# Optimization experiments

Hardware: AMD Instinct MI355X
Metric: run time of the kernel (lower is better)

The kernel has to match this reference:

```python
import jax, jax.numpy as jnp
import numpy as np

B, S, D = 32, 2048, 1024


def setup_inputs() -> dict:
    key = jax.random.key(0)
    k = jax.random.split(key, 7)
    midi_features = jax.random.normal(k[0], (B, S, D), dtype=jnp.float32)
    scale_id = jax.random.randint(k[1], (B,), 0, 3)
    midi_mask = jax.random.randint(k[2], (B, S), 0, 2).astype(jnp.int32)
    # Stacked branch params: index 0=high, 1=mid, 2=low (matches SCALE_TO_ID)
    W = jax.random.normal(k[3], (3, D, D), dtype=jnp.float32) * 0.02  # Linear weight (out,in)
    b = jax.random.normal(k[4], (3, D), dtype=jnp.float32) * 0.02
    scale_embed = jax.random.normal(k[5], (3, D), dtype=jnp.float32) * 0.02
    branch_embed = jax.random.normal(k[6], (3, D), dtype=jnp.float32) * 0.02
    return {"midi_features": midi_features, "scale_id": scale_id, "midi_mask": midi_mask,
            "W": W, "b": b, "scale_embed": scale_embed, "branch_embed": branch_embed}


def reference(midi_features, scale_id, midi_mask, W, b, scale_embed, branch_embed):
    # Per-sample scale routing: gather the branch's Linear weight for each sample
    # (equivalent to the torch fancy-indexing scatter into out[idx]).
    Wb = W[scale_id]               # (B, D, D) torch Linear convention: y = x @ W.T + b
    bb = b[scale_id]               # (B, D)
    out = jax.nn.silu(jnp.einsum('bsd,bed->bse', midi_features, Wb) + bb[:, None, :])
    # Dropout is identity in eval mode.
    out = out + scale_embed[scale_id][:, None, :]       # (B, S, D)

    seq_mask = midi_mask > 0                             # (B, S) bool
    w = seq_mask.astype(out.dtype)[:, :, None]           # (B, S, 1)
    denom = jnp.maximum(w.sum(axis=1), 1e-6)             # (B, 1)
    low_vec = (out * w).sum(axis=1) / denom              # (B, D) masked mean

    high_cond = out + branch_embed[0]                    # (B, S, D)
    mid_cond = out + branch_embed[1]                     # (B, S, D)
    low_cond = low_vec[:, None, :] + branch_embed[2]     # (B, 1, D) weak_low_alignment=True
    return high_cond, mid_cond, low_cond
```

## Files before the change

### kernel.cpp

```cpp
#include <hip/hip_runtime.h>
#include <hip/hip_bf16.h>

#define B_ 32
#define S_ 2048
#define D_ 1024
#define BM 128
#define BN 128
#define BK 64
#define NK (D_ / BK)

typedef __attribute__((ext_vector_type(8))) short bf16x8;
typedef __attribute__((ext_vector_type(4))) float f32x4;
typedef __attribute__((ext_vector_type(4))) float float4v;

#define AS1 __attribute__((address_space(1)))
#define AS3 __attribute__((address_space(3)))

__device__ __forceinline__ short f2bf(float f) {
    union { float f; unsigned u; } uf;
    uf.f = f;
    unsigned u = uf.u;
    u += 0x7FFFu + ((u >> 16) & 1u);
    return (short)(u >> 16);
}

__global__ __launch_bounds__(256) void cvt_bf16(const float4v* __restrict__ src,
                                                bf16x8* __restrict__ dst, int n8) {
    const int stride = gridDim.x * blockDim.x;
    for (int i = blockIdx.x * blockDim.x + threadIdx.x; i < n8; i += stride) {
        float4v a = src[2 * i], b = src[2 * i + 1];
        bf16x8 v;
#pragma unroll
        for (int j = 0; j < 4; ++j) {
            v[j]     = f2bf(a[j]);
            v[4 + j] = f2bf(b[j]);
        }
        dst[i] = v;
    }
}

__global__ __launch_bounds__(256, 2) void fused_gemm_bf16(
    const __hip_bfloat16* __restrict__ aBf,
    const __hip_bfloat16* __restrict__ wBf,
    const int*   __restrict__ scale_id,
    const int*   __restrict__ mask,
    const float* __restrict__ bias,
    const float* __restrict__ scemb,
    const float* __restrict__ bremb,
    float*       __restrict__ out,
    float*       __restrict__ colws)
{
    __shared__ __align__(16) short As[2][BM * BK];
    __shared__ __align__(16) short Bs[2][BM * BK];

    const int tid = threadIdx.x;
    const int lane = tid & 63;
    const int wid = tid >> 6;

    const int NTI = D_ / BN;
    const int MTI = S_ / BM;
    const int NWG = B_ * MTI * NTI;
    const int CPX = NWG / 8;
    int lid = ((int)blockIdx.x % 8) * CPX + ((int)blockIdx.x / 8);
    int nt = lid % NTI;
    int mt = (lid / NTI) % MTI;
    int bb = lid / (NTI * MTI);

    const int sid = scale_id[bb];

    const __hip_bfloat16* aBase = aBf + ((size_t)bb * S_ + (size_t)mt * BM) * D_;
    const __hip_bfloat16* bBase = wBf + ((size_t)sid * D_ + (size_t)nt * BN) * D_;

    const int l3 = lane >> 3;
    const int cb = (lane & 7) * 16;

    auto stage = [&](int buf, int kt) {
#pragma unroll
        for (int c = 0; c < 4; ++c) {
            const int seg = c * 4 + wid;
            const int row = seg * 8 + l3;
            const int scb = cb ^ ((row & 7) << 4);
            const __hip_bfloat16* ga = aBase + (size_t)row * D_ + kt * BK + (scb >> 1);
            const __hip_bfloat16* gb = bBase + (size_t)row * D_ + kt * BK + (scb >> 1);
            __builtin_amdgcn_global_load_lds((const AS1 unsigned int*)ga,
                (AS3 unsigned int*)&As[buf][seg * 512], 16, 0, 0);
            __builtin_amdgcn_global_load_lds((const AS1 unsigned int*)gb,
                (AS3 unsigned int*)&Bs[buf][seg * 512], 16, 0, 0);
        }
    };

    f32x4 acc[4][4];
#pragma unroll
    for (int mi = 0; mi < 4; ++mi)
#pragma unroll
        for (int ni = 0; ni < 4; ++ni)
            acc[mi][ni] = (f32x4){0.f, 0.f, 0.f, 0.f};

    const int wm = wid >> 1, wn = wid & 1;
    const int fr = lane & 15;
    const int fg = lane >> 4;

    stage(0, 0);
    asm volatile("s_waitcnt vmcnt(0)" ::: "memory");
    __syncthreads();

    int buf = 0;
    for (int kt = 0; kt < NK; ++kt) {
        if (kt + 1 < NK) stage(buf ^ 1, kt + 1);
#pragma unroll
        for (int kk = 0; kk < 2; ++kk) {
            bf16x8 af[4], bfr[4];
#pragma unroll
            for (int mi = 0; mi < 4; ++mi) {
                const int row = wm * 64 + mi * 16 + fr;
                const int byt = row * 128 + ((kk * 64 + fg * 16) ^ ((fr & 7) << 4));
                af[mi] = *(const bf16x8*)((const char*)&As[buf][0] + byt);
            }
#pragma unroll
            for (int ni = 0; ni < 4; ++ni) {
                const int row = wn * 64 + ni * 16 + fr;
                const int byt = row * 128 + ((kk * 64 + fg * 16) ^ ((fr & 7) << 4));
                bfr[ni] = *(const bf16x8*)((const char*)&Bs[buf][0] + byt);
            }
#pragma unroll
            for (int mi = 0; mi < 4; ++mi)
#pragma unroll
                for (int ni = 0; ni < 4; ++ni)
                    acc[mi][ni] = __builtin_amdgcn_mfma_f32_16x16x32_bf16(
                        af[mi], bfr[ni], acc[mi][ni], 0, 0, 0);
        }
        asm volatile("s_waitcnt vmcnt(0)" ::: "memory");
        __syncthreads();
        buf ^= 1;
    }

    const int ncolbase = nt * BN + wn * 64;
    float bv[4], sv[4];
#pragma unroll
    for (int ni = 0; ni < 4; ++ni) {
        const int n = ncolbase + ni * 16 + fr;
        bv[ni] = bias[sid * D_ + n];
        sv[ni] = scemb[sid * D_ + n];
    }

    float colsum[4] = {0.f, 0.f, 0.f, 0.f};
#pragma unroll
    for (int mi = 0; mi < 4; ++mi) {
        const int mrow0 = mt * BM + wm * 64 + mi * 16 + fg * 4;
        float mk[4];
#pragma unroll
        for (int r = 0; r < 4; ++r)
            mk[r] = (mask[(size_t)bb * S_ + mrow0 + r] > 0) ? 1.f : 0.f;
#pragma unroll
        for (int ni = 0; ni < 4; ++ni) {
#pragma unroll
            for (int r = 0; r < 4; ++r) {
                const float v = acc[mi][ni][r] + bv[ni];
                const float o = v / (1.f + __expf(-v)) + sv[ni];
                acc[mi][ni][r] = o;
                colsum[ni] += mk[r] * o;
            }
        }
    }

#pragma unroll
    for (int ni = 0; ni < 4; ++ni) {
        float s = colsum[ni];
        s += __shfl_xor(s, 16);
        s += __shfl_xor(s, 32);
        if (fg == 0)
            atomicAdd(&colws[(size_t)bb * D_ + (ncolbase + ni * 16 + fr)], s);
    }

    float* ldsF = (float*)&As[0][0];
    const int lrowR = tid >> 3;
    const int c8 = tid & 7;

    float4v b0q[4], b1q[4];
#pragma unroll
    for (int q = 0; q < 4; ++q) {
        const int gcol = nt * BN + (c8 + q * 8) * 4;
        b0q[q] = *(const float4v*)&bremb[0 * D_ + gcol];
        b1q[q] = *(const float4v*)&bremb[1 * D_ + gcol];
    }

    const size_t MIDOFF = (size_t)B_ * S_ * D_;

#pragma unroll
    for (int mi = 0; mi < 4; ++mi) {
#pragma unroll
        for (int ni = 0; ni < 4; ++ni)
#pragma unroll
            for (int r = 0; r < 4; ++r)
                ldsF[(wm * 16 + fg * 4 + r) * 132 + wn * 64 + ni * 16 + fr] =
                    acc[mi][ni][r];
        __syncthreads();

        const int grow = mt * BM + (lrowR >> 4) * 64 + mi * 16 + (lrowR & 15);
        const size_t rowbase = ((size_t)bb * S_ + grow) * D_ + nt * BN;
#pragma unroll
        for (int q = 0; q < 4; ++q) {
            const int c4 = c8 + q * 8;
            float4v v = *(const float4v*)&ldsF[lrowR * 132 + c4 * 4];
            float4v h = v + b0q[q];
            float4v m = v + b1q[q];
            __builtin_nontemporal_store(h, (float4v*)&out[rowbase + c4 * 4]);
            __builtin_nontemporal_store(m, (float4v*)&out[MIDOFF + rowbase + c4 * 4]);
        }
        __syncthreads();
    }
}

__global__ __launch_bounds__(256, 2) void fused_gemm_f32(
    const float* __restrict__ midi,
    const int*   __restrict__ scale_id,
    const int*   __restrict__ mask,
    const float* __restrict__ W,
    const float* __restrict__ bias,
    const float* __restrict__ scemb,
    const float* __restrict__ bremb,
    float*       __restrict__ out,
    float*       __restrict__ ws)
{
    __shared__ __align__(16) short As[BM * BK];
    __shared__ __align__(16) short Bs[BM * BK];

    const int tid = threadIdx.x;
    const int NTI = D_ / BN;
    const int MTI = S_ / BM;
    const int NWG = B_ * MTI * NTI;
    const int CPX = NWG / 8;
    int lid = ((int)blockIdx.x % 8) * CPX + ((int)blockIdx.x / 8);
    int nt = lid % NTI;
    int mt = (lid / NTI) % MTI;
    int bb = lid / (NTI * MTI);

    const int sid = scale_id[bb];
    const float* aBase = midi + ((size_t)bb * S_ + (size_t)mt * BM) * D_;
    const float* bBase = W + ((size_t)sid * D_ + (size_t)nt * BN) * D_;

    const int r0 = tid >> 3;
    const int kp = (tid & 7) * 8;

    float4v aL[4], aH[4], bL[4], bH[4];

    auto load_regs = [&](int kt) {
        const int kc = kt * BK + kp;
#pragma unroll
        for (int i = 0; i < 4; ++i) {
            const float* pa = aBase + (size_t)(r0 + 32 * i) * D_ + kc;
            aL[i] = *(const float4v*)pa;
            aH[i] = *(const float4v*)(pa + 4);
            const float* pb = bBase + (size_t)(r0 + 32 * i) * D_ + kc;
            bL[i] = *(const float4v*)pb;
            bH[i] = *(const float4v*)(pb + 4);
        }
    };

    auto write_lds = [&]() {
#pragma unroll
        for (int i = 0; i < 4; ++i) {
            const int row = r0 + 32 * i;
            const int off = (row * BK + kp) ^ ((row & 7) << 3);
            bf16x8 va, vb;
#pragma unroll
            for (int j = 0; j < 4; ++j) {
                va[j]     = f2bf(aL[i][j]);
                va[4 + j] = f2bf(aH[i][j]);
                vb[j]     = f2bf(bL[i][j]);
                vb[4 + j] = f2bf(bH[i][j]);
            }
            *(bf16x8*)&As[off] = va;
            *(bf16x8*)&Bs[off] = vb;
        }
    };

    f32x4 acc[4][4];
#pragma unroll
    for (int mi = 0; mi < 4; ++mi)
#pragma unroll
        for (int ni = 0; ni < 4; ++ni)
            acc[mi][ni] = (f32x4){0.f, 0.f, 0.f, 0.f};

    const int lane = tid & 63;
    const int wid = tid >> 6;
    const int wm = wid >> 1, wn = wid & 1;
    const int fr = lane & 15;
    const int fg = lane >> 4;

    load_regs(0);
    write_lds();
    __syncthreads();

    for (int kt = 0; kt < NK; ++kt) {
        if (kt + 1 < NK) load_regs(kt + 1);
#pragma unroll
        for (int kk = 0; kk < 2; ++kk) {
            bf16x8 af[4], bfr[4];
#pragma unroll
            for (int mi = 0; mi < 4; ++mi) {
                const int row = wm * 64 + mi * 16 + fr;
                const int off = (row * BK + kk * 32 + fg * 8) ^ ((row & 7) << 3);
                af[mi] = *(const bf16x8*)&As[off];
            }
#pragma unroll
            for (int ni = 0; ni < 4; ++ni) {
                const int row = wn * 64 + ni * 16 + fr;
                const int off = (row * BK + kk * 32 + fg * 8) ^ ((row & 7) << 3);
                bfr[ni] = *(const bf16x8*)&Bs[off];
            }
#pragma unroll
            for (int mi = 0; mi < 4; ++mi)
#pragma unroll
                for (int ni = 0; ni < 4; ++ni)
                    acc[mi][ni] = __builtin_amdgcn_mfma_f32_16x16x32_bf16(
                        af[mi], bfr[ni], acc[mi][ni], 0, 0, 0);
        }
        __syncthreads();
        if (kt + 1 < NK) write_lds();
        __syncthreads();
    }

    const int ncolbase = nt * BN + wn * 64;
    float bv[4], sv[4], b0v[4], b1v[4];
#pragma unroll
    for (int ni = 0; ni < 4; ++ni) {
        const int n = ncolbase + ni * 16 + fr;
        bv[ni]  = bias[sid * D_ + n];
        sv[ni]  = scemb[sid * D_ + n];
        b0v[ni] = bremb[0 * D_ + n];
        b1v[ni] = bremb[1 * D_ + n];
    }

    const size_t MIDOFF = (size_t)B_ * S_ * D_;
    float colsum[4] = {0.f, 0.f, 0.f, 0.f};

#pragma unroll
    for (int mi = 0; mi < 4; ++mi) {
        const int mrow0 = mt * BM + wm * 64 + mi * 16 + fg * 4;
        float mk[4];
#pragma unroll
        for (int r = 0; r < 4; ++r)
            mk[r] = (mask[(size_t)bb * S_ + mrow0 + r] > 0) ? 1.f : 0.f;
#pragma unroll
        for (int ni = 0; ni < 4; ++ni) {
            const int n = ncolbase + ni * 16 + fr;
#pragma unroll
            for (int r = 0; r < 4; ++r) {
                const float v = acc[mi][ni][r] + bv[ni];
                const float o = v / (1.f + __expf(-v)) + sv[ni];
                const size_t idx = ((size_t)bb * S_ + (size_t)(mrow0 + r)) * D_ + n;
                __builtin_nontemporal_store(o + b0v[ni], &out[idx]);
                __builtin_nontemporal_store(o + b1v[ni], &out[MIDOFF + idx]);
                colsum[ni] += mk[r] * o;
            }
        }
    }

#pragma unroll
    for (int ni = 0; ni < 4; ++ni) {
        float s = colsum[ni];
        s += __shfl_xor(s, 16);
        s += __shfl_xor(s, 32);
        if (fg == 0)
            atomicAdd(&ws[(size_t)bb * D_ + (ncolbase + ni * 16 + fr)], s);
    }
}

__global__ void finalize(const int* __restrict__ mask,
                         const float* __restrict__ ws,
                         const float* __restrict__ bremb,
                         float* __restrict__ out)
{
    const int b = blockIdx.x;
    const int tid = threadIdx.x;

    int c = 0;
    for (int s = tid; s < S_; s += 256)
        c += (mask[(size_t)b * S_ + s] > 0) ? 1 : 0;
#pragma unroll
    for (int m = 1; m < 64; m <<= 1)
        c += __shfl_xor(c, m);

    __shared__ int part[4];
    if ((tid & 63) == 0) part[tid >> 6] = c;
    __syncthreads();
    const float denom = fmaxf((float)(part[0] + part[1] + part[2] + part[3]), 1e-6f);
    const float inv = 1.f / denom;

    const size_t LOWOFF = (size_t)2 * B_ * S_ * D_;
    for (int e = tid; e < D_; e += 256)
        out[LOWOFF + (size_t)b * D_ + e] = ws[(size_t)b * D_ + e] * inv + bremb[2 * D_ + e];
}

extern "C" void kernel_launch(void* const* d_in, const int* in_sizes, int n_in,
                              void* d_out, int out_size, void* d_ws, size_t ws_size,
                              hipStream_t stream) {
    const float* midi     = (const float*)d_in[0];
    const int*   scale_id = (const int*)d_in[1];
    const int*   mask     = (const int*)d_in[2];
    const float* W        = (const float*)d_in[3];
    const float* bias     = (const float*)d_in[4];
    const float* scemb    = (const float*)d_in[5];
    const float* bremb    = (const float*)d_in[6];
    float* out = (float*)d_out;
    float* colws = (float*)d_ws;

    const size_t COLWS_B = (size_t)B_ * D_ * sizeof(float);
    const size_t WBF_B   = (size_t)3 * D_ * D_ * sizeof(short);
    const size_t ABF_B   = (size_t)B_ * S_ * D_ * sizeof(short);
    const size_t need    = COLWS_B + WBF_B + ABF_B;

    hipMemsetAsync(colws, 0, COLWS_B, stream);

    if (ws_size >= need) {
        __hip_bfloat16* wBf = (__hip_bfloat16*)((char*)d_ws + COLWS_B);
        __hip_bfloat16* aBf = (__hip_bfloat16*)((char*)d_ws + COLWS_B + WBF_B);
        cvt_bf16<<<dim3(2048), dim3(256), 0, stream>>>(
            (const float4v*)midi, (bf16x8*)aBf, (B_ * S_ * D_) / 8);
        cvt_bf16<<<dim3(512), dim3(256), 0, stream>>>(
            (const float4v*)W, (bf16x8*)wBf, (3 * D_ * D_) / 8);
        fused_gemm_bf16<<<dim3(B_ * (S_ / BM) * (D_ / BN)), dim3(256), 0, stream>>>(
            aBf, wBf, scale_id, mask, bias, scemb, bremb, out, colws);
    } else {
        fused_gemm_f32<<<dim3(B_ * (S_ / BM) * (D_ / BN)), dim3(256), 0, stream>>>(
            midi, scale_id, mask, W, bias, scemb, bremb, out, colws);
    }

    finalize<<<dim3(B_), dim3(256), 0, stream>>>(mask, colws, bremb, out);
}
```

Before: 382.5 us.

## Enlarge bf16 GEMM tile to 256x256 with 8 waves and half-tile staging pipeline

```diff
diff --git a/kernel.cpp b/kernel.cpp
--- a/kernel.cpp
+++ b/kernel.cpp
@@ -4,10 +4,11 @@
 #define B_ 32
 #define S_ 2048
 #define D_ 1024
-#define BM 128
-#define BN 128
+
+#define BM 256
+#define BN 256
 #define BK 64
-#define NK (D_ / BK)
+#define NKT (D_ / BK)
 
 typedef __attribute__((ext_vector_type(8))) short bf16x8;
 typedef __attribute__((ext_vector_type(4))) float f32x4;
@@ -39,7 +40,7 @@
     }
 }
 
-__global__ __launch_bounds__(256, 2) void fused_gemm_bf16(
+__global__ __launch_bounds__(512, 2) void fused_gemm_bf16(
     const __hip_bfloat16* __restrict__ aBf,
     const __hip_bfloat16* __restrict__ wBf,
     const int*   __restrict__ scale_id,
@@ -56,6 +57,8 @@
     const int tid = threadIdx.x;
     const int lane = tid & 63;
     const int wid = tid >> 6;
+    const int wm = wid >> 2;
+    const int wn = wid & 3;
 
     const int NTI = D_ / BN;
     const int MTI = S_ / BM;
@@ -67,119 +70,150 @@
     int bb = lid / (NTI * MTI);
 
     const int sid = scale_id[bb];
-
     const __hip_bfloat16* aBase = aBf + ((size_t)bb * S_ + (size_t)mt * BM) * D_;
     const __hip_bfloat16* bBase = wBf + ((size_t)sid * D_ + (size_t)nt * BN) * D_;
 
-    const int l3 = lane >> 3;
-    const int cb = (lane & 7) * 16;
-
-    auto stage = [&](int buf, int kt) {
-#pragma unroll
-        for (int c = 0; c < 4; ++c) {
-            const int seg = c * 4 + wid;
-            const int row = seg * 8 + l3;
-            const int scb = cb ^ ((row & 7) << 4);
-            const __hip_bfloat16* ga = aBase + (size_t)row * D_ + kt * BK + (scb >> 1);
-            const __hip_bfloat16* gb = bBase + (size_t)row * D_ + kt * BK + (scb >> 1);
-            __builtin_amdgcn_global_load_lds((const AS1 unsigned int*)ga,
-                (AS3 unsigned int*)&As[buf][seg * 512], 16, 0, 0);
-            __builtin_amdgcn_global_load_lds((const AS1 unsigned int*)gb,
-                (AS3 unsigned int*)&Bs[buf][seg * 512], 16, 0, 0);
+    const int lrow8 = lane >> 3;
+    const int scb = ((lane & 7) * 16) ^ (lrow8 << 4);
+
+    auto stageA = [&](int nb, int h, int kt) {
+#pragma unroll
+        for (int j = 0; j < 2; ++j) {
+            const int base = h * 128 + j * 64 + wid * 8;
+            const int grow = j * 128 + h * 64 + wid * 8 + lrow8;
+            const __hip_bfloat16* g = aBase + (size_t)grow * D_ + kt * BK + (scb >> 1);
+            __builtin_amdgcn_global_load_lds((const AS1 unsigned int*)g,
+                (AS3 unsigned int*)&As[nb][base * 64], 16, 0, 0);
         }
     };
-
-    f32x4 acc[4][4];
-#pragma unroll
-    for (int mi = 0; mi < 4; ++mi)
+    auto stageB = [&](int nb, int h, int kt) {
+#pragma unroll
+        for (int j = 0; j < 2; ++j) {
+            const int base = h * 128 + j * 64 + wid * 8;
+            const int grow = base + lrow8;
+            const __hip_bfloat16* g = bBase + (size_t)grow * D_ + kt * BK + (scb >> 1);
+            __builtin_amdgcn_global_load_lds((const AS1 unsigned int*)g,
+                (AS3 unsigned int*)&Bs[nb][base * 64], 16, 0, 0);
+        }
+    };
+
+    const int fr = lane & 15;
+    const int fg = lane >> 4;
+
+    f32x4 acc[8][4];
+#pragma unroll
+    for (int mi = 0; mi < 8; ++mi)
 #pragma unroll
         for (int ni = 0; ni < 4; ++ni)
             acc[mi][ni] = (f32x4){0.f, 0.f, 0.f, 0.f};
 
-    const int wm = wid >> 1, wn = wid & 1;
-    const int fr = lane & 15;
-    const int fg = lane >> 4;
-
-    stage(0, 0);
-    asm volatile("s_waitcnt vmcnt(0)" ::: "memory");
+    auto compute = [&](int cur, int mh, int bh) {
+        bf16x8 af[4][2], bv[2][2];
+#pragma unroll
+        for (int mi = 0; mi < 4; ++mi) {
+            const int l = mh * 128 + wm * 64 + mi * 16 + fr;
+            const int rb = l * 128;
+#pragma unroll
+            for (int kk = 0; kk < 2; ++kk) {
+                const int byt = rb + ((kk * 64 + fg * 16) ^ ((l & 7) << 4));
+                af[mi][kk] = *(const bf16x8*)((const char*)&As[cur][0] + byt);
+            }
+        }
+#pragma unroll
+        for (int ni = 0; ni < 2; ++ni) {
+            const int l = bh * 128 + wn * 32 + ni * 16 + fr;
+            const int rb = l * 128;
+#pragma unroll
+            for (int kk = 0; kk < 2; ++kk) {
+                const int byt = rb + ((kk * 64 + fg * 16) ^ ((l & 7) << 4));
+                bv[ni][kk] = *(const bf16x8*)((const char*)&Bs[cur][0] + byt);
+            }
+        }
+        __builtin_amdgcn_s_setprio(1);
+#pragma unroll
+        for (int mi = 0; mi < 4; ++mi)
+#pragma unroll
+            for (int ni = 0; ni < 2; ++ni)
+#pragma unroll
+                for (int kk = 0; kk < 2; ++kk)
+                    acc[mh * 4 + mi][bh * 2 + ni] = __builtin_amdgcn_mfma_f32_16x16x32_bf16(
+                        af[mi][kk], bv[ni][kk], acc[mh * 4 + mi][bh * 2 + ni], 0, 0, 0);
+        __builtin_amdgcn_s_setprio(0);
+    };
+
+#define PWAIT() do { \
+    asm volatile("s_waitcnt vmcnt(6)" ::: "memory"); \
+    asm volatile("s_barrier" ::: "memory"); } while (0)
+
+    stageB(0, 0, 0); stageA(0, 0, 0); stageB(0, 1, 0); stageA(0, 1, 0);
+
+    for (int kt = 0; kt < NKT; kt += 2) {
+        const int k1 = kt + 1;
+        const int k1n = (k1 + 1 < NKT) ? k1 + 1 : k1;
+        stageB(1, 0, k1);  PWAIT(); compute(0, 0, 0);
+        stageA(1, 0, k1);  PWAIT(); compute(0, 0, 1);
+        stageB(1, 1, k1);  PWAIT(); compute(0, 1, 0);
+        stageA(1, 1, k1);  PWAIT(); compute(0, 1, 1);
+        stageB(0, 0, k1n); PWAIT(); compute(1, 0, 0);
+        stageA(0, 0, k1n); PWAIT(); compute(1, 0, 1);
+        stageB(0, 1, k1n); PWAIT(); compute(1, 1, 0);
+        stageA(0, 1, k1n); PWAIT(); compute(1, 1, 1);
+    }
+#undef PWAIT
+
     __syncthreads();
 
-    int buf = 0;
-    for (int kt = 0; kt < NK; ++kt) {
-        if (kt + 1 < NK) stage(buf ^ 1, kt + 1);
-#pragma unroll
-        for (int kk = 0; kk < 2; ++kk) {
-            bf16x8 af[4], bfr[4];
-#pragma unroll
-            for (int mi = 0; mi < 4; ++mi) {
-                const int row = wm * 64 + mi * 16 + fr;
-                const int byt = row * 128 + ((kk * 64 + fg * 16) ^ ((fr & 7) << 4));
-                af[mi] = *(const bf16x8*)((const char*)&As[buf][0] + byt);
-            }
-#pragma unroll
-            for (int ni = 0; ni < 4; ++ni) {
-                const int row = wn * 64 + ni * 16 + fr;
-                const int byt = row * 128 + ((kk * 64 + fg * 16) ^ ((fr & 7) << 4));
-                bfr[ni] = *(const bf16x8*)((const char*)&Bs[buf][0] + byt);
-            }
-#pragma unroll
-            for (int mi = 0; mi < 4; ++mi)
-#pragma unroll
-                for (int ni = 0; ni < 4; ++ni)
-                    acc[mi][ni] = __builtin_amdgcn_mfma_f32_16x16x32_bf16(
-                        af[mi], bfr[ni], acc[mi][ni], 0, 0, 0);
-        }
-        asm volatile("s_waitcnt vmcnt(0)" ::: "memory");
-        __syncthreads();
-        buf ^= 1;
-    }
-
-    const int ncolbase = nt * BN + wn * 64;
-    float bv[4], sv[4];
-#pragma unroll
-    for (int ni = 0; ni < 4; ++ni) {
-        const int n = ncolbase + ni * 16 + fr;
-        bv[ni] = bias[sid * D_ + n];
-        sv[ni] = scemb[sid * D_ + n];
-    }
-
-    float colsum[4] = {0.f, 0.f, 0.f, 0.f};
-#pragma unroll
-    for (int mi = 0; mi < 4; ++mi) {
-        const int mrow0 = mt * BM + wm * 64 + mi * 16 + fg * 4;
+    const int colb = nt * BN;
+    float bv2[2][2], sv2[2][2];
+#pragma unroll
+    for (int bh = 0; bh < 2; ++bh)
+#pragma unroll
+        for (int ni = 0; ni < 2; ++ni) {
+            const int n = colb + bh * 128 + wn * 32 + ni * 16 + fr;
+            bv2[bh][ni] = bias[sid * D_ + n];
+            sv2[bh][ni] = scemb[sid * D_ + n];
+        }
+
+    float colsum[2][2] = {{0.f, 0.f}, {0.f, 0.f}};
+#pragma unroll
+    for (int mig = 0; mig < 8; ++mig) {
+        const int mrow0 = mt * BM + wm * 128 + mig * 16 + fg * 4;
         float mk[4];
 #pragma unroll
         for (int r = 0; r < 4; ++r)
             mk[r] = (mask[(size_t)bb * S_ + mrow0 + r] > 0) ? 1.f : 0.f;
 #pragma unroll
-        for (int ni = 0; ni < 4; ++ni) {
-#pragma unroll
-            for (int r = 0; r < 4; ++r) {
-                const float v = acc[mi][ni][r] + bv[ni];
-                const float o = v / (1.f + __expf(-v)) + sv[ni];
-                acc[mi][ni][r] = o;
-                colsum[ni] += mk[r] * o;
-            }
-        }
-    }
-
-#pragma unroll
-    for (int ni = 0; ni < 4; ++ni) {
-        float s = colsum[ni];
-        s += __shfl_xor(s, 16);
-        s += __shfl_xor(s, 32);
-        if (fg == 0)
-            atomicAdd(&colws[(size_t)bb * D_ + (ncolbase + ni * 16 + fr)], s);
-    }
+        for (int bh = 0; bh < 2; ++bh)
+#pragma unroll
+            for (int ni = 0; ni < 2; ++ni)
+#pragma unroll
+                for (int r = 0; r < 4; ++r) {
+                    const float v = acc[mig][bh * 2 + ni][r] + bv2[bh][ni];
+                    const float o = v / (1.f + __expf(-v)) + sv2[bh][ni];
+                    acc[mig][bh * 2 + ni][r] = o;
+                    colsum[bh][ni] += mk[r] * o;
+                }
+    }
+
+#pragma unroll
+    for (int bh = 0; bh < 2; ++bh)
+#pragma unroll
+        for (int ni = 0; ni < 2; ++ni) {
+            float s = colsum[bh][ni];
+            s += __shfl_xor(s, 16);
+            s += __shfl_xor(s, 32);
+            if (fg == 0)
+                atomicAdd(&colws[(size_t)bb * D_ + (colb + bh * 128 + wn * 32 + ni * 16 + fr)], s);
+        }
 
     float* ldsF = (float*)&As[0][0];
-    const int lrowR = tid >> 3;
-    const int c8 = tid & 7;
+    const int lr = tid >> 4;
+    const int cg = tid & 15;
 
     float4v b0q[4], b1q[4];
 #pragma unroll
     for (int q = 0; q < 4; ++q) {
-        const int gcol = nt * BN + (c8 + q * 8) * 4;
+        const int gcol = colb + cg * 16 + q * 4;
         b0q[q] = *(const float4v*)&bremb[0 * D_ + gcol];
         b1q[q] = *(const float4v*)&bremb[1 * D_ + gcol];
     }
@@ -187,29 +221,36 @@
     const size_t MIDOFF = (size_t)B_ * S_ * D_;
 
 #pragma unroll
-    for (int mi = 0; mi < 4; ++mi) {
-#pragma unroll
-        for (int ni = 0; ni < 4; ++ni)
-#pragma unroll
-            for (int r = 0; r < 4; ++r)
-                ldsF[(wm * 16 + fg * 4 + r) * 132 + wn * 64 + ni * 16 + fr] =
-                    acc[mi][ni][r];
+    for (int mig = 0; mig < 8; ++mig) {
+#pragma unroll
+        for (int bh = 0; bh < 2; ++bh)
+#pragma unroll
+            for (int ni = 0; ni < 2; ++ni)
+#pragma unroll
+                for (int r = 0; r < 4; ++r)
+                    ldsF[(wm * 16 + fg * 4 + r) * 260 + bh * 128 + wn * 32 + ni * 16 + fr] =
+                        acc[mig][bh * 2 + ni][r];
         __syncthreads();
 
-        const int grow = mt * BM + (lrowR >> 4) * 64 + mi * 16 + (lrowR & 15);
-        const size_t rowbase = ((size_t)bb * S_ + grow) * D_ + nt * BN;
+        const int grow = mt * BM + (lr >> 4) * 128 + mig * 16 + (lr & 15);
+        const size_t rowbase = ((size_t)bb * S_ + grow) * D_ + colb;
 #pragma unroll
         for (int q = 0; q < 4; ++q) {
-            const int c4 = c8 + q * 8;
-            float4v v = *(const float4v*)&ldsF[lrowR * 132 + c4 * 4];
+            const int c0 = cg * 16 + q * 4;
+            float4v v = *(const float4v*)&ldsF[lr * 260 + c0];
             float4v h = v + b0q[q];
             float4v m = v + b1q[q];
-            __builtin_nontemporal_store(h, (float4v*)&out[rowbase + c4 * 4]);
-            __builtin_nontemporal_store(m, (float4v*)&out[MIDOFF + rowbase + c4 * 4]);
+            __builtin_nontemporal_store(h, (float4v*)&out[rowbase + c0]);
+            __builtin_nontemporal_store(m, (float4v*)&out[MIDOFF + rowbase + c0]);
         }
         __syncthreads();
     }
 }
+
+#define FBM 128
+#define FBN 128
+#define FBK 64
+#define FNK (D_ / FBK)
 
 __global__ __launch_bounds__(256, 2) void fused_gemm_f32(
     const float* __restrict__ midi,
@@ -222,12 +263,12 @@
     float*       __restrict__ out,
     float*       __restrict__ ws)
 {
-    __shared__ __align__(16) short As[BM * BK];
-    __shared__ __align__(16) short Bs[BM * BK];
+    __shared__ __align__(16) short As[FBM * FBK];
+    __shared__ __align__(16) short Bs[FBM * FBK];
 
     const int tid = threadIdx.x;
-    const int NTI = D_ / BN;
-    const int MTI = S_ / BM;
+    const int NTI = D_ / FBN;
+    const int MTI = S_ / FBM;
     const int NWG = B_ * MTI * NTI;
     const int CPX = NWG / 8;
     int lid = ((int)blockIdx.x % 8) * CPX + ((int)blockIdx.x / 8);
@@ -236,8 +277,8 @@
     int bb = lid / (NTI * MTI);
 
     const int sid = scale_id[bb];
-    const float* aBase = midi + ((size_t)bb * S_ + (size_t)mt * BM) * D_;
-    const float* bBase = W + ((size_t)sid * D_ + (size_t)nt * BN) * D_;
+    const float* aBase = midi + ((size_t)bb * S_ + (size_t)mt * FBM) * D_;
+    const float* bBase = W + ((size_t)sid * D_ + (size_t)nt * FBN) * D_;
 
     const int r0 = tid >> 3;
     const int kp = (tid & 7) * 8;
@@ -245,7 +286,7 @@
     float4v aL[4], aH[4], bL[4], bH[4];
 
     auto load_regs = [&](int kt) {
-        const int kc = kt * BK + kp;
+        const int kc = kt * FBK + kp;
 #pragma unroll
         for (int i = 0; i < 4; ++i) {
             const float* pa = aBase + (size_t)(r0 + 32 * i) * D_ + kc;
@@ -261,7 +302,7 @@
 #pragma unroll
         for (int i = 0; i < 4; ++i) {
             const int row = r0 + 32 * i;
-            const int off = (row * BK + kp) ^ ((row & 7) << 3);
+            const int off = (row * FBK + kp) ^ ((row & 7) << 3);
             bf16x8 va, vb;
 #pragma unroll
             for (int j = 0; j < 4; ++j) {
@@ -292,21 +333,21 @@
     write_lds();
     __syncthreads();
 
-    for (int kt = 0; kt < NK; ++kt) {
-        if (kt + 1 < NK) load_regs(kt + 1);
+    for (int kt = 0; kt < FNK; ++kt) {
+        if (kt + 1 < FNK) load_regs(kt + 1);
 #pragma unroll
         for (int kk = 0; kk < 2; ++kk) {
             bf16x8 af[4], bfr[4];
 #pragma unroll
             for (int mi = 0; mi < 4; ++mi) {
                 const int row = wm * 64 + mi * 16 + fr;
-                const int off = (row * BK + kk * 32 + fg * 8) ^ ((row & 7) << 3);
+                const int off = (row * FBK + kk * 32 + fg * 8) ^ ((row & 7) << 3);
                 af[mi] = *(const bf16x8*)&As[off];
             }
 #pragma unroll
             for (int ni = 0; ni < 4; ++ni) {
                 const int row = wn * 64 + ni * 16 + fr;
-                const int off = (row * BK + kk * 32 + fg * 8) ^ ((row & 7) << 3);
+                const int off = (row * FBK + kk * 32 + fg * 8) ^ ((row & 7) << 3);
                 bfr[ni] = *(const bf16x8*)&Bs[off];
             }
 #pragma unroll
@@ -317,11 +358,11 @@
                         af[mi], bfr[ni], acc[mi][ni], 0, 0, 0);
         }
         __syncthreads();
-        if (kt + 1 < NK) write_lds();
+        if (kt + 1 < FNK) write_lds();
         __syncthreads();
     }
 
-    const int ncolbase = nt * BN + wn * 64;
+    const int ncolbase = nt * FBN + wn * 64;
     float bv[4], sv[4], b0v[4], b1v[4];
 #pragma unroll
     for (int ni = 0; ni < 4; ++ni) {
@@ -337,7 +378,7 @@
 
 #pragma unroll
     for (int mi = 0; mi < 4; ++mi) {
-        const int mrow0 = mt * BM + wm * 64 + mi * 16 + fg * 4;
+        const int mrow0 = mt * FBM + wm * 64 + mi * 16 + fg * 4;
         float mk[4];
 #pragma unroll
         for (int r = 0; r < 4; ++r)
@@ -420,10 +461,10 @@
             (const float4v*)midi, (bf16x8*)aBf, (B_ * S_ * D_) / 8);
         cvt_bf16<<<dim3(512), dim3(256), 0, stream>>>(
             (const float4v*)W, (bf16x8*)wBf, (3 * D_ * D_) / 8);
-        fused_gemm_bf16<<<dim3(B_ * (S_ / BM) * (D_ / BN)), dim3(256), 0, stream>>>(
+        fused_gemm_bf16<<<dim3(B_ * (S_ / BM) * (D_ / BN)), dim3(512), 0, stream>>>(
             aBf, wBf, scale_id, mask, bias, scemb, bremb, out, colws);
     } else {
-        fused_gemm_f32<<<dim3(B_ * (S_ / BM) * (D_ / BN)), dim3(256), 0, stream>>>(
+        fused_gemm_f32<<<dim3(B_ * (S_ / FBM) * (D_ / FBN)), dim3(256), 0, stream>>>(
             midi, scale_id, mask, W, bias, scemb, bremb, out, colws);
     }
 
```

After: 1.038 ms. 171% more time.
